# Performance work log

Measured on AMD Instinct MI355X. Metric: run time of the kernel, lower is better.

## Reference

```python
import jax, jax.numpy as jnp
import numpy as np

B, C, D = 2048, 1000, 256


def setup_inputs() -> dict:
    key = jax.random.key(0)
    k1, k2 = jax.random.split(key)
    x = jax.random.normal(k1, (B, D), dtype=jnp.float32)
    # xavier_uniform for prototypes [C, D]: bound = sqrt(6 / (C + D))
    bound = np.sqrt(6.0 / (C + D)).astype(np.float32)
    prototypes = jax.random.uniform(k2, (C, D), dtype=jnp.float32,
                                    minval=-bound, maxval=bound)
    log_diag = jnp.zeros((C, D), dtype=jnp.float32)
    return {"x": x, "prototypes": prototypes, "log_diag": log_diag}


def reference(x, prototypes, log_diag):
    # diff: [B, C, D] broadcast of x against class prototypes
    diff = x[:, None, :] - prototypes[None, :, :]
    precision_diag = jnp.exp(log_diag)  # [C, D]
    # per-class diagonal-weighted squared distance, reduced over features
    mahalanobis_sq = jnp.sum(diff * diff * precision_diag[None, :, :], axis=2)  # [B, C]
    return -mahalanobis_sq
```

## Files before the change

kernel.cpp:

```cpp
#include <hip/hip_runtime.h>
#include <hip/hip_bf16.h>


#define C_N 1000
#define D_N 256

typedef __attribute__((ext_vector_type(8))) short bf16x8;
typedef __attribute__((ext_vector_type(4))) float f32x4;

__device__ inline bf16x8 pack8(const float* v) {
  union { bf16x8 o; __hip_bfloat162 h[4]; } u;
#pragma unroll
  for (int j = 0; j < 4; ++j)
    u.h[j] = __float22bfloat162_rn(make_float2(v[2 * j], v[2 * j + 1]));
  return u.o;
}

__global__ __launch_bounds__(512, 2) void mahal_fused(
    const float* __restrict__ x, const float* __restrict__ p,
    const float* __restrict__ ld, float* __restrict__ out) {
  __shared__ short lA[8][8][64][8];
  __shared__ short lB[4][16][64][8];
  __shared__ float s_lds[2][64];

  const int tid = threadIdx.x;
  const int w   = tid >> 6;
  const int l   = tid & 63;
  const int r16 = l & 15;
  const int hi  = l >> 4;
  const int bx  = blockIdx.x;
  const int by  = blockIdx.y;

  bf16x8 xa_sv[8];

  {
    const int ct = w & 3;
    const int dh = w >> 2;
    const int c  = by * 64 + ct * 16 + r16;
    const bool valid = (c < C_N);
    float sp = 0.f;
#pragma unroll
    for (int t = 0; t < 4; ++t) {
      const int d = dh * 128 + t * 32 + hi * 8;
      float wv[8], pwv[8];
      if (valid) {
        const float* lp = ld + (size_t)c * D_N + d;
        const float* pp = p  + (size_t)c * D_N + d;
        float4 l0 = *reinterpret_cast<const float4*>(lp);
        float4 l1 = *reinterpret_cast<const float4*>(lp + 4);
        float4 p0 = *reinterpret_cast<const float4*>(pp);
        float4 p1 = *reinterpret_cast<const float4*>(pp + 4);
        float lv[8] = {l0.x,l0.y,l0.z,l0.w,l1.x,l1.y,l1.z,l1.w};
        float pv[8] = {p0.x,p0.y,p0.z,p0.w,p1.x,p1.y,p1.z,p1.w};
#pragma unroll
        for (int j = 0; j < 8; ++j) {
          float wj = __expf(lv[j]);
          wv[j]  = wj;
          pwv[j] = -2.f * pv[j] * wj;
          sp += pv[j] * pv[j] * wj;
        }
      } else {
#pragma unroll
        for (int j = 0; j < 8; ++j) { wv[j] = 0.f; pwv[j] = 0.f; }
      }
      *reinterpret_cast<bf16x8*>(&lB[ct][dh * 4 + t][l][0])     = pack8(wv);
      *reinterpret_cast<bf16x8*>(&lB[ct][8 + dh * 4 + t][l][0]) = pack8(pwv);
    }
    sp += __shfl_xor(sp, 16, 64);
    sp += __shfl_xor(sp, 32, 64);
    if (l < 16) s_lds[dh][ct * 16 + r16] = sp;
  }

  {
    const int row = bx * 128 + w * 16 + r16;
#pragma unroll
    for (int t = 0; t < 8; ++t) {
      const int d = t * 32 + hi * 8;
      const float* xp = x + (size_t)row * D_N + d;
      float4 v0 = *reinterpret_cast<const float4*>(xp);
      float4 v1 = *reinterpret_cast<const float4*>(xp + 4);
      float v[8] = {v0.x,v0.y,v0.z,v0.w,v1.x,v1.y,v1.z,v1.w};
      float sq[8];
#pragma unroll
      for (int j = 0; j < 8; ++j) sq[j] = v[j] * v[j];
      *reinterpret_cast<bf16x8*>(&lA[w][t][l][0]) = pack8(sq);
      xa_sv[t] = pack8(v);
    }
  }
  __syncthreads();

  const int wm = w >> 1, wn = w & 1;
  f32x4 acc[2][2];
#pragma unroll
  for (int i = 0; i < 2; ++i)
#pragma unroll
    for (int jn = 0; jn < 2; ++jn) acc[i][jn] = {0.f, 0.f, 0.f, 0.f};

#pragma unroll
  for (int kt = 0; kt < 8; ++kt) {
    bf16x8 a0 = *reinterpret_cast<const bf16x8*>(&lA[wm * 2 + 0][kt][l][0]);
    bf16x8 a1 = *reinterpret_cast<const bf16x8*>(&lA[wm * 2 + 1][kt][l][0]);
    bf16x8 b0 = *reinterpret_cast<const bf16x8*>(&lB[wn * 2 + 0][kt][l][0]);
    bf16x8 b1 = *reinterpret_cast<const bf16x8*>(&lB[wn * 2 + 1][kt][l][0]);
    acc[0][0] = __builtin_amdgcn_mfma_f32_16x16x32_bf16(a0, b0, acc[0][0], 0, 0, 0);
    acc[0][1] = __builtin_amdgcn_mfma_f32_16x16x32_bf16(a0, b1, acc[0][1], 0, 0, 0);
    acc[1][0] = __builtin_amdgcn_mfma_f32_16x16x32_bf16(a1, b0, acc[1][0], 0, 0, 0);
    acc[1][1] = __builtin_amdgcn_mfma_f32_16x16x32_bf16(a1, b1, acc[1][1], 0, 0, 0);
  }
  __syncthreads();

#pragma unroll
  for (int t = 0; t < 8; ++t)
    *reinterpret_cast<bf16x8*>(&lA[w][t][l][0]) = xa_sv[t];
  __syncthreads();

#pragma unroll
  for (int kt = 0; kt < 8; ++kt) {
    bf16x8 a0 = *reinterpret_cast<const bf16x8*>(&lA[wm * 2 + 0][kt][l][0]);
    bf16x8 a1 = *reinterpret_cast<const bf16x8*>(&lA[wm * 2 + 1][kt][l][0]);
    bf16x8 b0 = *reinterpret_cast<const bf16x8*>(&lB[wn * 2 + 0][8 + kt][l][0]);
    bf16x8 b1 = *reinterpret_cast<const bf16x8*>(&lB[wn * 2 + 1][8 + kt][l][0]);
    acc[0][0] = __builtin_amdgcn_mfma_f32_16x16x32_bf16(a0, b0, acc[0][0], 0, 0, 0);
    acc[0][1] = __builtin_amdgcn_mfma_f32_16x16x32_bf16(a0, b1, acc[0][1], 0, 0, 0);
    acc[1][0] = __builtin_amdgcn_mfma_f32_16x16x32_bf16(a1, b0, acc[1][0], 0, 0, 0);
    acc[1][1] = __builtin_amdgcn_mfma_f32_16x16x32_bf16(a1, b1, acc[1][1], 0, 0, 0);
  }

  const int colbase = by * 64 + wn * 32 + r16;
  const int rowbase = bx * 128 + wm * 32 + hi * 4;
#pragma unroll
  for (int jn = 0; jn < 2; ++jn) {
    const int col = colbase + jn * 16;
    if (col < C_N) {
      const int ci = wn * 32 + jn * 16 + r16;
      const float sc = s_lds[0][ci] + s_lds[1][ci];
#pragma unroll
      for (int i = 0; i < 2; ++i) {
        const int row = rowbase + i * 16;
#pragma unroll
        for (int r = 0; r < 4; ++r)
          out[(size_t)(row + r) * C_N + col] = -(acc[i][jn][r] + sc);
      }
    }
  }
}

extern "C" void kernel_launch(void* const* d_in, const int* in_sizes, int n_in,
                              void* d_out, int out_size, void* d_ws, size_t ws_size,
                              hipStream_t stream) {
  const float* x  = (const float*)d_in[0];
  const float* p  = (const float*)d_in[1];
  const float* ld = (const float*)d_in[2];
  float* out = (float*)d_out;
  mahal_fused<<<dim3(16, 16), 512, 0, stream>>>(x, p, ld, out);
}
```

Before: 17.04 us.

## Keep A fragments in registers and drop the A LDS staging

Each wave now keeps its own 16 rows of x (squared and raw, as bf16) in registers and computes all 64 columns. The A tile no longer goes through shared memory, which removes two block barriers and the LDS round trip for A. Two independent accumulator sets (squared-term and cross-term) are kept and summed only at the end, which improves MFMA independence. In exchange, each wave now reads the full B tile from LDS, and register pressure rises from the extra accumulators and the 16 held A fragments.

```diff
diff --git a/kernel.cpp b/kernel.cpp
--- a/kernel.cpp
+++ b/kernel.cpp
@@ -19,7 +19,6 @@
 __global__ __launch_bounds__(512, 2) void mahal_fused(
     const float* __restrict__ x, const float* __restrict__ p,
     const float* __restrict__ ld, float* __restrict__ out) {
-  __shared__ short lA[8][8][64][8];
   __shared__ short lB[4][16][64][8];
   __shared__ float s_lds[2][64];
 
@@ -30,8 +29,6 @@
   const int hi  = l >> 4;
   const int bx  = blockIdx.x;
   const int by  = blockIdx.y;
-
-  bf16x8 xa_sv[8];
 
   {
     const int ct = w & 3;
@@ -71,6 +68,7 @@
     if (l < 16) s_lds[dh][ct * 16 + r16] = sp;
   }
 
+  bf16x8 aSq[8], aRaw[8];
   {
     const int row = bx * 128 + w * 16 + r16;
 #pragma unroll
@@ -83,64 +81,37 @@
       float sq[8];
 #pragma unroll
       for (int j = 0; j < 8; ++j) sq[j] = v[j] * v[j];
-      *reinterpret_cast<bf16x8*>(&lA[w][t][l][0]) = pack8(sq);
-      xa_sv[t] = pack8(v);
+      aSq[t]  = pack8(sq);
+      aRaw[t] = pack8(v);
     }
   }
   __syncthreads();
 
-  const int wm = w >> 1, wn = w & 1;
-  f32x4 acc[2][2];
+  f32x4 acc0[4], acc1[4];
 #pragma unroll
-  for (int i = 0; i < 2; ++i)
-#pragma unroll
-    for (int jn = 0; jn < 2; ++jn) acc[i][jn] = {0.f, 0.f, 0.f, 0.f};
+  for (int n = 0; n < 4; ++n) { acc0[n] = {0.f,0.f,0.f,0.f}; acc1[n] = {0.f,0.f,0.f,0.f}; }
 
 #pragma unroll
   for (int kt = 0; kt < 8; ++kt) {
-    bf16x8 a0 = *reinterpret_cast<const bf16x8*>(&lA[wm * 2 + 0][kt][l][0]);
-    bf16x8 a1 = *reinterpret_cast<const bf16x8*>(&lA[wm * 2 + 1][kt][l][0]);
-    bf16x8 b0 = *reinterpret_cast<const bf16x8*>(&lB[wn * 2 + 0][kt][l][0]);
-    bf16x8 b1 = *reinterpret_cast<const bf16x8*>(&lB[wn * 2 + 1][kt][l][0]);
-    acc[0][0] = __builtin_amdgcn_mfma_f32_16x16x32_bf16(a0, b0, acc[0][0], 0, 0, 0);
-    acc[0][1] = __builtin_amdgcn_mfma_f32_16x16x32_bf16(a0, b1, acc[0][1], 0, 0, 0);
-    acc[1][0] = __builtin_amdgcn_mfma_f32_16x16x32_bf16(a1, b0, acc[1][0], 0, 0, 0);
-    acc[1][1] = __builtin_amdgcn_mfma_f32_16x16x32_bf16(a1, b1, acc[1][1], 0, 0, 0);
-  }
-  __syncthreads();
-
 #pragma unroll
-  for (int t = 0; t < 8; ++t)
-    *reinterpret_cast<bf16x8*>(&lA[w][t][l][0]) = xa_sv[t];
-  __syncthreads();
-
-#pragma unroll
-  for (int kt = 0; kt < 8; ++kt) {
-    bf16x8 a0 = *reinterpret_cast<const bf16x8*>(&lA[wm * 2 + 0][kt][l][0]);
-    bf16x8 a1 = *reinterpret_cast<const bf16x8*>(&lA[wm * 2 + 1][kt][l][0]);
-    bf16x8 b0 = *reinterpret_cast<const bf16x8*>(&lB[wn * 2 + 0][8 + kt][l][0]);
-    bf16x8 b1 = *reinterpret_cast<const bf16x8*>(&lB[wn * 2 + 1][8 + kt][l][0]);
-    acc[0][0] = __builtin_amdgcn_mfma_f32_16x16x32_bf16(a0, b0, acc[0][0], 0, 0, 0);
-    acc[0][1] = __builtin_amdgcn_mfma_f32_16x16x32_bf16(a0, b1, acc[0][1], 0, 0, 0);
-    acc[1][0] = __builtin_amdgcn_mfma_f32_16x16x32_bf16(a1, b0, acc[1][0], 0, 0, 0);
-    acc[1][1] = __builtin_amdgcn_mfma_f32_16x16x32_bf16(a1, b1, acc[1][1], 0, 0, 0);
+    for (int n = 0; n < 4; ++n) {
+      bf16x8 b0 = *reinterpret_cast<const bf16x8*>(&lB[n][kt][l][0]);
+      bf16x8 b1 = *reinterpret_cast<const bf16x8*>(&lB[n][8 + kt][l][0]);
+      acc0[n] = __builtin_amdgcn_mfma_f32_16x16x32_bf16(aSq[kt],  b0, acc0[n], 0, 0, 0);
+      acc1[n] = __builtin_amdgcn_mfma_f32_16x16x32_bf16(aRaw[kt], b1, acc1[n], 0, 0, 0);
+    }
   }
 
-  const int colbase = by * 64 + wn * 32 + r16;
-  const int rowbase = bx * 128 + wm * 32 + hi * 4;
+  const int rowbase = bx * 128 + w * 16 + hi * 4;
 #pragma unroll
-  for (int jn = 0; jn < 2; ++jn) {
-    const int col = colbase + jn * 16;
+  for (int n = 0; n < 4; ++n) {
+    const int col = by * 64 + n * 16 + r16;
     if (col < C_N) {
-      const int ci = wn * 32 + jn * 16 + r16;
+      const int ci = n * 16 + r16;
       const float sc = s_lds[0][ci] + s_lds[1][ci];
 #pragma unroll
-      for (int i = 0; i < 2; ++i) {
-        const int row = rowbase + i * 16;
-#pragma unroll
-        for (int r = 0; r < 4; ++r)
-          out[(size_t)(row + r) * C_N + col] = -(acc[i][jn][r] + sc);
-      }
+      for (int r = 0; r < 4; ++r)
+        out[(size_t)(rowbase + r) * C_N + col] = -(acc0[n][r] + acc1[n][r] + sc);
     }
   }
 }
```

Result: faster. 16.09 us, median of 3 (-5.6%).
